# Kernel optimization log

Hardware: AMD Instinct MI355X
Metric: run time of the kernel (lower is better)

Reference implementation:

```python
import jax, jax.numpy as jnp
import numpy as np

N = 100000
E = 1600000
C_IN = 32
HEADS = 4
C = 32          # per-head out channels
L = 3           # num layers = num_hidden_layers + 1
NEG_SLOPE = 0.2


def setup_inputs() -> dict:
    key = jax.random.key(0)
    ks = jax.random.split(key, 8)
    x = jax.random.normal(ks[0], (N, C_IN), dtype=jnp.float32)
    edge_index = jax.random.randint(ks[1], (2, E), 0, N, dtype=jnp.int64)
    edge_attr = jax.random.normal(ks[2], (E, 8), dtype=jnp.float32)  # unused by GATConv (edge_dim=None)
    scale = 1.0 / np.sqrt(C_IN)
    Ws = jax.random.normal(ks[3], (L, C_IN, HEADS * C), dtype=jnp.float32) * scale
    att_src = jax.random.normal(ks[4], (L, HEADS, C), dtype=jnp.float32) * scale
    att_dst = jax.random.normal(ks[5], (L, HEADS, C), dtype=jnp.float32) * scale
    bias = jnp.zeros((L, C), dtype=jnp.float32)
    return {"x": x, "edge_index": edge_index, "edge_attr": edge_attr,
            "Ws": Ws, "att_src": att_src, "att_dst": att_dst, "bias": bias}


def _gat_layer(x, src, dst, W, a_src, a_dst, b):
    # x: [N, C_in]; src/dst: [E'] (self-loops included); W: [C_in, H*C]
    h = (x @ W).reshape(N, HEADS, C)                      # [N, H, C]
    alpha_src = jnp.sum(h * a_src, axis=-1)               # [N, H]
    alpha_dst = jnp.sum(h * a_dst, axis=-1)               # [N, H]
    e = alpha_src[src] + alpha_dst[dst]                   # [E', H]
    e = jnp.where(e > 0, e, NEG_SLOPE * e)                # leaky_relu
    # segment softmax over incoming edges of each dst node
    m = jax.ops.segment_max(e, dst, num_segments=N)       # [N, H]
    ex = jnp.exp(e - m[dst])
    s = jax.ops.segment_sum(ex, dst, num_segments=N)      # [N, H]
    alpha = ex / (s[dst] + 1e-16)                         # [E', H]
    msg = h[src] * alpha[:, :, None]                      # [E', H, C]
    out = jax.ops.segment_sum(msg, dst, num_segments=N)   # [N, H, C]
    return out.mean(axis=1) + b                           # concat=False -> mean over heads, + bias


def reference(x, edge_index, edge_attr, Ws, att_src, att_dst, bias):
    # add self loops once (GATConv add_self_loops=True)
    loops = jnp.arange(N, dtype=edge_index.dtype)
    src = jnp.concatenate([edge_index[0], loops])
    dst = jnp.concatenate([edge_index[1], loops])
    # edge_attr unused: GATConv built without edge_dim.
    # Dropout layers are identity in eval mode.
    for l in range(L):
        x = _gat_layer(x, src, dst, Ws[l], att_src[l], att_dst[l], bias[l])
        x = jax.nn.elu(x)
    return x
```

## Files before the change

kernel.cpp:

```cpp
#include <hip/hip_runtime.h>
#include <hip/hip_bf16.h>
#include <hip/hip_fp16.h>
#include <cstdint>


__global__ void k_scan1(const int* __restrict__ deg, int n, int* __restrict__ bsums) {
    __shared__ int s[256];
    int t = threadIdx.x;
    int i = blockIdx.x * 256 + t;
    int v = (i < n) ? deg[i] : 0;
    s[t] = v; __syncthreads();
    for (int off = 128; off > 0; off >>= 1) {
        if (t < off) s[t] += s[t + off];
        __syncthreads();
    }
    if (t == 0) bsums[blockIdx.x] = s[0];
}

__global__ void k_scan2(const int* __restrict__ bsums, int nb, int* __restrict__ boffs) {
    __shared__ int s[512];
    int t = threadIdx.x;
    int v = (t < nb) ? bsums[t] : 0;
    s[t] = v; __syncthreads();
    for (int off = 1; off < 512; off <<= 1) {
        int nv = (t >= off) ? s[t - off] : 0;
        __syncthreads();
        s[t] += nv;
        __syncthreads();
    }
    if (t < nb) boffs[t] = s[t] - v;
}

__global__ void k_scan3(const int* __restrict__ deg, int n, const int* __restrict__ boffs,
                        int* __restrict__ rowst) {
    __shared__ int s[256];
    int t = threadIdx.x;
    int i = blockIdx.x * 256 + t;
    int v = (i < n) ? deg[i] : 0;
    s[t] = v; __syncthreads();
    for (int off = 1; off < 256; off <<= 1) {
        int nv = (t >= off) ? s[t - off] : 0;
        __syncthreads();
        s[t] += nv;
        __syncthreads();
    }
    int incl = s[t] + boffs[blockIdx.x];
    if (i < n) {
        rowst[i] = incl - v;
        if (i == n - 1) rowst[n] = incl;
    }
}

__global__ void k_scatter(const int* __restrict__ src, const int* __restrict__ dst,
                          const int* __restrict__ rank, const int* __restrict__ rowst,
                          int E, int* __restrict__ col) {
    int t = blockIdx.x * blockDim.x + threadIdx.x;
    int base = t * 16;
    if (base + 16 <= E) {
        int4 d[4], s[4], r[4];
#pragma unroll
        for (int k = 0; k < 4; ++k) {
            d[k] = *reinterpret_cast<const int4*>(dst + base + k * 4);
            s[k] = *reinterpret_cast<const int4*>(src + base + k * 4);
            r[k] = *reinterpret_cast<const int4*>(rank + base + k * 4);
        }
        const int* dd = reinterpret_cast<const int*>(d);
        const int* ss = reinterpret_cast<const int*>(s);
        const int* rr = reinterpret_cast<const int*>(r);
        int p[16];
#pragma unroll
        for (int k = 0; k < 16; ++k) p[k] = rowst[dd[k]] + rr[k];
#pragma unroll
        for (int k = 0; k < 16; ++k) col[p[k]] = ss[k];
    } else {
        for (int i = base; i < E; ++i) col[rowst[dst[i]] + rank[i]] = src[i];
    }
}


__device__ __forceinline__ float lane_bcast(float v, int k) {
    return __int_as_float(__builtin_amdgcn_readlane(__float_as_int(v), k));
}

__global__ void __launch_bounds__(256)
k_gemm_alpha(const float* __restrict__ x, const float* __restrict__ W,
             const float* __restrict__ a_src, const float* __restrict__ a_dst,
             __half* __restrict__ h16, float* __restrict__ alpha_src,
             float* __restrict__ alpha_dst, int n,
             const int* __restrict__ dstv, int E, int* __restrict__ deg,
             int* __restrict__ rank, int gemmBlocks) {
    if ((int)blockIdx.x >= gemmBlocks) {
        int b = blockIdx.x - gemmBlocks;
        int base = (b * 256 + threadIdx.x) * 32;
        if (base + 32 <= E) {
            int4 d[8];
#pragma unroll
            for (int k = 0; k < 8; ++k)
                d[k] = *reinterpret_cast<const int4*>(dstv + base + k * 4);
            const int* dd = reinterpret_cast<const int*>(d);
            int r[32];
#pragma unroll
            for (int k = 0; k < 32; ++k) r[k] = atomicAdd(&deg[dd[k]], 1);
#pragma unroll
            for (int k = 0; k < 8; ++k)
                *reinterpret_cast<int4*>(rank + base + k * 4) =
                    *reinterpret_cast<const int4*>(r + k * 4);
        } else {
            for (int i = base; i < E; ++i) rank[i] = atomicAdd(&deg[dstv[i]], 1);
        }
        return;
    }
    int lane = threadIdx.x & 63;
    int wave = threadIdx.x >> 6;
    int j2 = lane * 2;
    int nbase = blockIdx.x * 64 + wave * 16;

    float2 wr[32];
#pragma unroll
    for (int k = 0; k < 32; ++k)
        wr[k] = *reinterpret_cast<const float2*>(W + k * 128 + j2);
    float2 as2 = *reinterpret_cast<const float2*>(a_src + j2);
    float2 ad2 = *reinterpret_cast<const float2*>(a_dst + j2);

    float xr[16];
#pragma unroll
    for (int m = 0; m < 16; ++m) {
        int node = nbase + m;
        xr[m] = (node < n) ? x[(size_t)node * 32 + (lane & 31)] : 0.f;
    }

#pragma unroll
    for (int m = 0; m < 16; ++m) {
        int node = nbase + m;
        if (node >= n) continue;
        float acc0 = 0.f, acc1 = 0.f;
#pragma unroll
        for (int k = 0; k < 32; ++k) {
            float xv = lane_bcast(xr[m], k);
            acc0 += xv * wr[k].x;
            acc1 += xv * wr[k].y;
        }
        *reinterpret_cast<__half2*>(h16 + (size_t)node * 128 + j2) =
            __floats2half2_rn(acc0, acc1);
        float ps = acc0 * as2.x + acc1 * as2.y;
        float pd = acc0 * ad2.x + acc1 * ad2.y;
#pragma unroll
        for (int mm = 1; mm < 16; mm <<= 1) {
            ps += __shfl_xor(ps, mm, 64);
            pd += __shfl_xor(pd, mm, 64);
        }
        if ((lane & 15) == 0) {
            int head = lane >> 4;
            alpha_src[node * 4 + head] = ps;
            alpha_dst[node * 4 + head] = pd;
        }
    }
}

__device__ __forceinline__ float lrelu_exp(float e) {
    e = e > 0.f ? e : 0.2f * e;
    return __expf(e);
}

__global__ void k_agg(const __half* __restrict__ h16, const float* __restrict__ asrc,
                      const float* __restrict__ adst, const int* __restrict__ rowst,
                      const int* __restrict__ col, const float* __restrict__ bias,
                      float* __restrict__ out, int n) {
    int wid = (int)((blockIdx.x * (size_t)blockDim.x + threadIdx.x) >> 6);
    if (wid >= n) return;
    int lane = threadIdx.x & 63;
    int g = lane >> 4;
    int q = lane & 15;
    int head = q >> 2;
    float ad = adst[wid * 4 + head];

    float acc[8] = {0.f, 0.f, 0.f, 0.f, 0.f, 0.f, 0.f, 0.f};
    float s = 0.f;

    if (g == 0) {
        float w = lrelu_exp(asrc[wid * 4 + head] + ad);
        uint4 v = *reinterpret_cast<const uint4*>(h16 + (size_t)wid * 128 + q * 8);
        const __half2* hp = reinterpret_cast<const __half2*>(&v);
        s = w;
#pragma unroll
        for (int k = 0; k < 4; ++k) {
            float2 f = __half22float2(hp[k]);
            acc[2 * k]     += w * f.x;
            acc[2 * k + 1] += w * f.y;
        }
    }

    int beg = rowst[wid], end = rowst[wid + 1];
    int i = beg + g;
    for (; i + 4 < end; i += 8) {
        int s0 = col[i];
        int s1 = col[i + 4];
        float x0 = asrc[s0 * 4 + head];
        float x1 = asrc[s1 * 4 + head];
        uint4 v0 = *reinterpret_cast<const uint4*>(h16 + (size_t)s0 * 128 + q * 8);
        uint4 v1 = *reinterpret_cast<const uint4*>(h16 + (size_t)s1 * 128 + q * 8);
        float w0 = lrelu_exp(x0 + ad);
        float w1 = lrelu_exp(x1 + ad);
        s += w0 + w1;
        const __half2* h0 = reinterpret_cast<const __half2*>(&v0);
        const __half2* h1 = reinterpret_cast<const __half2*>(&v1);
#pragma unroll
        for (int k = 0; k < 4; ++k) {
            float2 f0 = __half22float2(h0[k]);
            float2 f1 = __half22float2(h1[k]);
            acc[2 * k]     += w0 * f0.x + w1 * f1.x;
            acc[2 * k + 1] += w0 * f0.y + w1 * f1.y;
        }
    }
    if (i < end) {
        int s0 = col[i];
        float w = lrelu_exp(asrc[s0 * 4 + head] + ad);
        uint4 v = *reinterpret_cast<const uint4*>(h16 + (size_t)s0 * 128 + q * 8);
        const __half2* hp = reinterpret_cast<const __half2*>(&v);
        s += w;
#pragma unroll
        for (int k = 0; k < 4; ++k) {
            float2 f = __half22float2(hp[k]);
            acc[2 * k]     += w * f.x;
            acc[2 * k + 1] += w * f.y;
        }
    }

    s += __shfl_xor(s, 16, 64);
    s += __shfl_xor(s, 32, 64);
#pragma unroll
    for (int k = 0; k < 8; ++k) {
        acc[k] += __shfl_xor(acc[k], 16, 64);
        acc[k] += __shfl_xor(acc[k], 32, 64);
    }
    float inv = 1.f / s;
#pragma unroll
    for (int k = 0; k < 8; ++k) acc[k] *= inv;
#pragma unroll
    for (int k = 0; k < 8; ++k) {
        acc[k] += __shfl_xor(acc[k], 4, 64);
        acc[k] += __shfl_xor(acc[k], 8, 64);
    }
    if (lane < 4) {
        float o[8];
#pragma unroll
        for (int k = 0; k < 8; ++k) {
            float v = acc[k] * 0.25f + bias[lane * 8 + k];
            o[k] = v > 0.f ? v : (__expf(v) - 1.f);
        }
        float4* op = reinterpret_cast<float4*>(&out[(size_t)wid * 32 + lane * 8]);
        op[0] = make_float4(o[0], o[1], o[2], o[3]);
        op[1] = make_float4(o[4], o[5], o[6], o[7]);
    }
}


extern "C" void kernel_launch(void* const* d_in, const int* in_sizes, int n_in,
                              void* d_out, int out_size, void* d_ws, size_t ws_size,
                              hipStream_t stream) {
    const float* x       = (const float*)d_in[0];
    const int*   ei      = (const int*)d_in[1];
    const float* Ws      = (const float*)d_in[3];
    const float* att_src = (const float*)d_in[4];
    const float* att_dst = (const float*)d_in[5];
    const float* bias    = (const float*)d_in[6];

    int N = in_sizes[0] / 32;
    int E = in_sizes[1] / 2;
    const int* srcv = ei;
    const int* dstv = ei + E;

    float* fws   = (float*)d_ws;
    __half* h16  = (__half*)fws;
    float* asrc  = (float*)(h16 + (size_t)N * 128);
    float* adst  = asrc + (size_t)N * 4;
    float* xbuf  = adst + (size_t)N * 4;
    int*   deg    = (int*)(xbuf + (size_t)N * 32);
    int*   rowst  = deg + N;
    int*   bsums  = rowst + N + 1;
    int*   boffs  = bsums + 512;
    int*   col    = boffs + 512;
    int*   rank   = col + E;

    int nb256 = (N + 255) / 256;
    int gemmBlocks = (N + 63) / 64;
    int histBlocks = (E + 32 * 256 - 1) / (32 * 256);
    int scatBlocks = (E + 16 * 256 - 1) / (16 * 256);

    hipMemsetAsync(deg, 0, (size_t)N * sizeof(int), stream);

    for (int l = 0; l < 3; ++l) {
        const float* xin = (l == 0) ? x : xbuf;
        float* xout = (l == 2) ? (float*)d_out : xbuf;
        int extra = (l == 0) ? histBlocks : 0;
        k_gemm_alpha<<<gemmBlocks + extra, 256, 0, stream>>>(
            xin, Ws + (size_t)l * 32 * 128, att_src + l * 128, att_dst + l * 128,
            h16, asrc, adst, N, dstv, E, deg, rank, gemmBlocks);
        if (l == 0) {
            k_scan1<<<nb256, 256, 0, stream>>>(deg, N, bsums);
            k_scan2<<<1, 512, 0, stream>>>(bsums, nb256, boffs);
            k_scan3<<<nb256, 256, 0, stream>>>(deg, N, boffs, rowst);
            k_scatter<<<scatBlocks, 256, 0, stream>>>(srcv, dstv, rank, rowst, E, col);
        }
        k_agg<<<(N + 3) / 4, 256, 0, stream>>>(
            h16, asrc, adst, rowst, col, bias + l * 32, xout, N);
    }
}
```

Before: 426.5 us.

## Build CSR degree histogram with LDS-privatized per-chunk counts instead of global atomics

Replaces the global-atomic degree histogram, which was fused into the first GEMM launch, with a two-level scheme. Each block covers one edge chunk and one node range and counts in LDS. A per-node column scan over the chunks then produces the chunk offsets and degrees, and the scatter adds each chunk's offset to the rank. This targets contention on global atomics, but each block now reads its full edge chunk once per node range (8x the reads of dst), and there is an extra 32xN histogram buffer plus one more kernel launch.

New measurement: 452.6 us. 1.06x slower.

```diff
diff --git a/kernel.cpp b/kernel.cpp
--- a/kernel.cpp
+++ b/kernel.cpp
@@ -3,6 +3,47 @@
 #include <hip/hip_fp16.h>
 #include <cstdint>
 
+#define NCHUNK 32
+#define NRANGE 8
+#define SCAT_PER 16
+
+
+__global__ void __launch_bounds__(256)
+k_hist_lds(const int* __restrict__ dstv, int E, int chunkSize, int n, int rangeSize,
+           int* __restrict__ chist, int* __restrict__ rank) {
+    __shared__ int lh[12800];
+    int c = blockIdx.x & (NCHUNK - 1);
+    int r = blockIdx.x / NCHUNK;
+    int base = r * rangeSize;
+    int rsz = min(rangeSize, n - base);
+    if (rsz <= 0) return;
+    int t = threadIdx.x;
+    for (int i = t; i < rsz; i += 256) lh[i] = 0;
+    __syncthreads();
+    int e0 = c * chunkSize;
+    int e1 = min(e0 + chunkSize, E);
+    for (int i = e0 + t; i < e1; i += 256) {
+        int d = dstv[i];
+        unsigned rel = (unsigned)(d - base);
+        if (rel < (unsigned)rsz) rank[i] = atomicAdd(&lh[rel], 1);
+    }
+    __syncthreads();
+    int* out = chist + (size_t)c * n + base;
+    for (int i = t; i < rsz; i += 256) out[i] = lh[i];
+}
+
+__global__ void k_chist_scan(int* __restrict__ chist, int n, int* __restrict__ deg) {
+    int d = blockIdx.x * blockDim.x + threadIdx.x;
+    if (d >= n) return;
+    int sum = 0;
+#pragma unroll
+    for (int c = 0; c < NCHUNK; ++c) {
+        int v = chist[(size_t)c * n + d];
+        chist[(size_t)c * n + d] = sum;
+        sum += v;
+    }
+    deg[d] = sum;
+}
 
 __global__ void k_scan1(const int* __restrict__ deg, int n, int* __restrict__ bsums) {
     __shared__ int s[256];
@@ -53,10 +94,15 @@
 
 __global__ void k_scatter(const int* __restrict__ src, const int* __restrict__ dst,
                           const int* __restrict__ rank, const int* __restrict__ rowst,
-                          int E, int* __restrict__ col) {
-    int t = blockIdx.x * blockDim.x + threadIdx.x;
-    int base = t * 16;
-    if (base + 16 <= E) {
+                          const int* __restrict__ chist, int n, int E, int chunkSize,
+                          int blocksPerChunk, int* __restrict__ col) {
+    int c = blockIdx.x / blocksPerChunk;
+    int lb = blockIdx.x % blocksPerChunk;
+    const int* cslice = chist + (size_t)c * n;
+    int cbeg = c * chunkSize;
+    int cend = min(cbeg + chunkSize, E);
+    int base = cbeg + (lb * 256 + threadIdx.x) * SCAT_PER;
+    if (base + SCAT_PER <= cend) {
         int4 d[4], s[4], r[4];
 #pragma unroll
         for (int k = 0; k < 4; ++k) {
@@ -69,11 +115,12 @@
         const int* rr = reinterpret_cast<const int*>(r);
         int p[16];
 #pragma unroll
-        for (int k = 0; k < 16; ++k) p[k] = rowst[dd[k]] + rr[k];
+        for (int k = 0; k < 16; ++k) p[k] = rowst[dd[k]] + cslice[dd[k]] + rr[k];
 #pragma unroll
         for (int k = 0; k < 16; ++k) col[p[k]] = ss[k];
     } else {
-        for (int i = base; i < E; ++i) col[rowst[dst[i]] + rank[i]] = src[i];
+        for (int i = base; i < cend; ++i)
+            col[rowst[dst[i]] + cslice[dst[i]] + rank[i]] = src[i];
     }
 }
 
@@ -86,30 +133,7 @@
 k_gemm_alpha(const float* __restrict__ x, const float* __restrict__ W,
              const float* __restrict__ a_src, const float* __restrict__ a_dst,
              __half* __restrict__ h16, float* __restrict__ alpha_src,
-             float* __restrict__ alpha_dst, int n,
-             const int* __restrict__ dstv, int E, int* __restrict__ deg,
-             int* __restrict__ rank, int gemmBlocks) {
-    if ((int)blockIdx.x >= gemmBlocks) {
-        int b = blockIdx.x - gemmBlocks;
-        int base = (b * 256 + threadIdx.x) * 32;
-        if (base + 32 <= E) {
-            int4 d[8];
-#pragma unroll
-            for (int k = 0; k < 8; ++k)
-                d[k] = *reinterpret_cast<const int4*>(dstv + base + k * 4);
-            const int* dd = reinterpret_cast<const int*>(d);
-            int r[32];
-#pragma unroll
-            for (int k = 0; k < 32; ++k) r[k] = atomicAdd(&deg[dd[k]], 1);
-#pragma unroll
-            for (int k = 0; k < 8; ++k)
-                *reinterpret_cast<int4*>(rank + base + k * 4) =
-                    *reinterpret_cast<const int4*>(r + k * 4);
-        } else {
-            for (int i = base; i < E; ++i) rank[i] = atomicAdd(&deg[dstv[i]], 1);
-        }
-        return;
-    }
+             float* __restrict__ alpha_dst, int n) {
     int lane = threadIdx.x & 63;
     int wave = threadIdx.x >> 6;
     int j2 = lane * 2;
@@ -281,27 +305,29 @@
     int*   boffs  = bsums + 512;
     int*   col    = boffs + 512;
     int*   rank   = col + E;
+    int*   chist  = rank + E;
 
     int nb256 = (N + 255) / 256;
     int gemmBlocks = (N + 63) / 64;
-    int histBlocks = (E + 32 * 256 - 1) / (32 * 256);
-    int scatBlocks = (E + 16 * 256 - 1) / (16 * 256);
-
-    hipMemsetAsync(deg, 0, (size_t)N * sizeof(int), stream);
+    int rangeSize = (N + NRANGE - 1) / NRANGE;
+    int chunkSize = (E + NCHUNK - 1) / NCHUNK;
+    int blocksPerChunk = (chunkSize + 256 * SCAT_PER - 1) / (256 * SCAT_PER);
+
+    k_hist_lds<<<NRANGE * NCHUNK, 256, 0, stream>>>(dstv, E, chunkSize, N, rangeSize,
+                                                    chist, rank);
+    k_chist_scan<<<nb256, 256, 0, stream>>>(chist, N, deg);
+    k_scan1<<<nb256, 256, 0, stream>>>(deg, N, bsums);
+    k_scan2<<<1, 512, 0, stream>>>(bsums, nb256, boffs);
+    k_scan3<<<nb256, 256, 0, stream>>>(deg, N, boffs, rowst);
+    k_scatter<<<NCHUNK * blocksPerChunk, 256, 0, stream>>>(
+        srcv, dstv, rank, rowst, chist, N, E, chunkSize, blocksPerChunk, col);
 
     for (int l = 0; l < 3; ++l) {
         const float* xin = (l == 0) ? x : xbuf;
         float* xout = (l == 2) ? (float*)d_out : xbuf;
-        int extra = (l == 0) ? histBlocks : 0;
-        k_gemm_alpha<<<gemmBlocks + extra, 256, 0, stream>>>(
+        k_gemm_alpha<<<gemmBlocks, 256, 0, stream>>>(
             xin, Ws + (size_t)l * 32 * 128, att_src + l * 128, att_dst + l * 128,
-            h16, asrc, adst, N, dstv, E, deg, rank, gemmBlocks);
-        if (l == 0) {
-            k_scan1<<<nb256, 256, 0, stream>>>(deg, N, bsums);
-            k_scan2<<<1, 512, 0, stream>>>(bsums, nb256, boffs);
-            k_scan3<<<nb256, 256, 0, stream>>>(deg, N, boffs, rowst);
-            k_scatter<<<scatBlocks, 256, 0, stream>>>(srcv, dstv, rank, rowst, E, col);
-        }
+            h16, asrc, adst, N);
         k_agg<<<(N + 3) / 4, 256, 0, stream>>>(
             h16, asrc, adst, rowst, col, bias + l * 32, xout, N);
     }
```
